# Kernel optimization log

Measured on AMD Instinct MI355X. Metric: run time of the kernel, lower is better.

## Reference

```python
import jax, jax.numpy as jnp
import numpy as np

V, D, H, L, FF, B, S = 32000, 1024, 16, 4, 4096, 2, 1024
DK = D // H
STD = 0.02


def setup_inputs() -> dict:
    key = jax.random.key(0)
    ks = jax.random.split(key, 9)
    emb = jax.random.normal(ks[0], (V, D), jnp.float32) * STD
    w_qkv = jax.random.normal(ks[1], (L, D, 3 * D), jnp.float32) * STD
    w_o = jax.random.normal(ks[2], (L, D, D), jnp.float32) * STD
    w_gate = jax.random.normal(ks[3], (L, D, FF), jnp.float32) * STD
    w_up = jax.random.normal(ks[4], (L, D, FF), jnp.float32) * STD
    w_down = jax.random.normal(ks[5], (L, FF, D), jnp.float32) * STD
    norm1_w = jnp.ones((L, D), jnp.float32)
    norm2_w = jnp.ones((L, D), jnp.float32)
    final_norm_w = jnp.ones((D,), jnp.float32)
    input_ids = jax.random.randint(ks[6], (B, S), 0, V, dtype=jnp.int32)
    return dict(input_ids=input_ids, emb=emb, w_qkv=w_qkv, w_o=w_o,
                norm1_w=norm1_w, norm2_w=norm2_w,
                w_gate=w_gate, w_up=w_up, w_down=w_down,
                final_norm_w=final_norm_w)


def _rms(x, w, eps=1e-8):
    return w * x / jnp.sqrt(jnp.mean(x * x, axis=-1, keepdims=True) + eps)


def _rope_factor(seq_len, dk):
    # original: x_rope = x*cos + x*sin with cos/sin of shape [S, dk/2]
    # (duplicated along the feature dim to make the broadcast well-defined)
    pos = jnp.arange(seq_len, dtype=jnp.float32)
    freqs = jnp.exp(jnp.arange(0, dk, 2, dtype=jnp.float32) * (-jnp.log(10000.0) / dk))
    ang = pos[:, None] * freqs[None, :]                     # [S, dk/2]
    c = jnp.cos(ang); s = jnp.sin(ang)
    return jnp.concatenate([c, c], -1) + jnp.concatenate([s, s], -1)  # [S, dk]


def reference(input_ids, emb, w_qkv, w_o, norm1_w, norm2_w, w_gate, w_up, w_down, final_norm_w):
    b, s = input_ids.shape
    d = emb.shape[1]
    x = emb[input_ids] * jnp.sqrt(jnp.float32(d))           # [B,S,D]
    rope = _rope_factor(s, DK)                              # [S,DK]
    causal = jnp.tril(jnp.ones((s, s), bool))
    scale = 1.0 / jnp.sqrt(jnp.float32(DK))

    def block(x, p):
        wqkv, wo, n1, n2, wg, wu, wd = p
        nx = _rms(x, n1)
        qkv = (nx @ wqkv).reshape(b, s, 3, H, DK).transpose(2, 0, 3, 1, 4)  # [3,B,H,S,DK]
        q, k, v = qkv[0], qkv[1], qkv[2]
        q = q * rope
        k = k * rope
        scores = jnp.einsum('bhsd,bhtd->bhst', q, k) * scale
        scores = jnp.where(causal, scores, jnp.float32(-1e9))
        attn = jax.nn.softmax(scores, axis=-1)
        o = jnp.einsum('bhst,bhtd->bhsd', attn, v)
        o = o.transpose(0, 2, 1, 3).reshape(b, s, d)
        x = x + o @ wo
        nx = _rms(x, n2)
        ff = (jax.nn.silu(nx @ wg) * (nx @ wu)) @ wd
        return x + ff, None

    x, _ = jax.lax.scan(block, x, (w_qkv, w_o, norm1_w, norm2_w, w_gate, w_up, w_down))
    x = _rms(x, final_norm_w)
    logits = x @ emb.T                                      # tied lm_head
    return logits
```

## Files before the change

### kernel.cpp

```cpp
#include <hip/hip_runtime.h>
#include <hip/hip_bf16.h>
#include <math.h>

#define B_ 2
#define S_ 1024
#define D_ 1024
#define H_ 16
#define DK_ 64
#define L_ 4
#define FF_ 4096
#define V_ 32000
#define NT (B_*S_)

typedef __attribute__((ext_vector_type(8))) short short8v;
typedef __attribute__((ext_vector_type(4))) float floatx4;
typedef __hip_bfloat16 bf16;

__device__ inline float b2f(unsigned short u) {
  unsigned v = ((unsigned)u) << 16;
  float f; __builtin_memcpy(&f, &v, 4); return f;
}
__device__ inline unsigned short f2bu(float f) {
  bf16 h = __float2bfloat16(f);
  unsigned short u; __builtin_memcpy(&u, &h, 2); return u;
}

__global__ __launch_bounds__(256) void k_embed(const int* __restrict__ ids,
    const float* __restrict__ emb, float* __restrict__ x) {
  int i = blockIdx.x*256 + threadIdx.x;
  if (i >= NT*D_) return;
  int tok = i >> 10;
  int d = i & 1023;
  x[i] = emb[(size_t)ids[tok]*D_ + d] * 32.0f;
}

__global__ __launch_bounds__(256) void k_rms(const float* __restrict__ x,
    const float* __restrict__ w, bf16* __restrict__ o) {
  int row = blockIdx.x;
  const float* xr = x + (size_t)row*D_;
  float s = 0.f;
  for (int d = threadIdx.x; d < D_; d += 256) { float v = xr[d]; s += v*v; }
  for (int off = 32; off; off >>= 1) s += __shfl_down(s, off);
  __shared__ float red[4];
  __shared__ float inv_s;
  int wid = threadIdx.x >> 6;
  if ((threadIdx.x & 63) == 0) red[wid] = s;
  __syncthreads();
  if (threadIdx.x == 0) {
    float t = red[0]+red[1]+red[2]+red[3];
    inv_s = 1.0f / sqrtf(t * (1.0f/D_) + 1e-8f);
  }
  __syncthreads();
  float inv = inv_s;
  bf16* orow = o + (size_t)row*D_;
  for (int d = threadIdx.x; d < D_; d += 256) orow[d] = __float2bfloat16(w[d]*xr[d]*inv);
}

__global__ __launch_bounds__(256) void k_transpose_cast(const float* __restrict__ src0,
    bf16* __restrict__ dst0, int K, int N, size_t src_stride, size_t dst_stride) {
  const float* src = src0 + blockIdx.z * src_stride;
  bf16* dst = dst0 + blockIdx.z * dst_stride;
  __shared__ float t[64][65];
  int k0 = blockIdx.y*64, n0 = blockIdx.x*64;
  int r  = threadIdx.x >> 4;
  int c4 = (threadIdx.x & 15)*4;
  #pragma unroll
  for (int i = 0; i < 4; ++i) {
    float4 v = *(const float4*)(src + (size_t)(k0 + r + i*16)*N + n0 + c4);
    t[r+i*16][c4] = v.x; t[r+i*16][c4+1] = v.y;
    t[r+i*16][c4+2] = v.z; t[r+i*16][c4+3] = v.w;
  }
  __syncthreads();
  int nn = threadIdx.x >> 2;
  int kc = threadIdx.x & 3;
  #pragma unroll
  for (int i = 0; i < 4; ++i) {
    int kk = kc*4 + i*16;
    ushort4 o;
    o.x = f2bu(t[kk][nn]);   o.y = f2bu(t[kk+1][nn]);
    o.z = f2bu(t[kk+2][nn]); o.w = f2bu(t[kk+3][nn]);
    *(ushort4*)(dst + (size_t)(n0+nn)*K + k0 + kk) = o;
  }
}

__global__ __launch_bounds__(256) void k_cast4(const float* __restrict__ s,
    bf16* __restrict__ d, int n4) {
  int i = blockIdx.x*256 + threadIdx.x;
  if (i >= n4) return;
  float4 v = ((const float4*)s)[i];
  ushort4 o;
  o.x = f2bu(v.x); o.y = f2bu(v.y); o.z = f2bu(v.z); o.w = f2bu(v.w);
  ((ushort4*)d)[i] = o;
}

template<int EPI, bool OUTBF>
__global__ __launch_bounds__(256) void k_mfma_gemm_bt(
    const bf16* __restrict__ A, const bf16* __restrict__ Bt,
    const void* __restrict__ aux, void* __restrict__ Cout,
    int M, int N, int K) {
  const int NM = M >> 7, NN = N >> 7;
  const int wg = blockIdx.x;
  const int grp = wg >> 3, xcd = wg & 7;
  const int mi = grp % NM;
  const int ni = xcd + 8*(grp / NM);
  if (ni >= NN) return;
  const int bm = mi * 128;
  const int bn = ni * 128;

  __shared__ bf16 As[128*32];
  __shared__ bf16 Bs[128*32];
  const int tid  = threadIdx.x;
  const int lane = tid & 63;
  const int wave = tid >> 6;
  const int wm = (wave >> 1) * 64;
  const int wn = (wave & 1) * 64;

  floatx4 acc[4][4] = {};

  for (int k0 = 0; k0 < K; k0 += 32) {
    #pragma unroll
    for (int c = 0; c < 2; ++c) {
      int e = (c*256 + tid) * 8;
      int row = e >> 5, col = e & 31;
      const bf16* ga = A  + (size_t)(bm + row)*K + k0 + col;
      const bf16* gb = Bt + (size_t)(bn + row)*K + k0 + col;
      int ldsoff = (c*256 + wave*64) * 8;
      __builtin_amdgcn_global_load_lds(
        (const __attribute__((address_space(1))) void*)ga,
        (__attribute__((address_space(3))) void*)(As + ldsoff), 16, 0, 0);
      __builtin_amdgcn_global_load_lds(
        (const __attribute__((address_space(1))) void*)gb,
        (__attribute__((address_space(3))) void*)(Bs + ldsoff), 16, 0, 0);
    }
    __syncthreads();
    const int r = lane & 15, kc = lane >> 4;
    short8v a[4], b[4];
    #pragma unroll
    for (int i = 0; i < 4; ++i) {
      a[i] = *(const short8v*)(As + (size_t)(wm + i*16 + r)*32 + kc*8);
      b[i] = *(const short8v*)(Bs + (size_t)(wn + i*16 + r)*32 + kc*8);
    }
    #pragma unroll
    for (int i = 0; i < 4; ++i)
      #pragma unroll
      for (int j = 0; j < 4; ++j)
        acc[i][j] = __builtin_amdgcn_mfma_f32_16x16x32_bf16(a[i], b[j], acc[i][j], 0, 0, 0);
    __syncthreads();
  }

  const int cn = lane & 15, rq = lane >> 4;
  #pragma unroll
  for (int i=0;i<4;i++) {
    #pragma unroll
    for (int j=0;j<4;j++) {
      const int gcol = bn + wn + j*16 + cn;
      float freq = 0.f;
      if constexpr (EPI==2) {
        if (gcol < 2048)
          freq = expf((float)(gcol & 31) * -0.28782313662425574f);
      }
      #pragma unroll
      for (int rr=0; rr<4; ++rr) {
        const int grow = bm + wm + i*16 + rq*4 + rr;
        const size_t off = (size_t)grow*N + gcol;
        float v = acc[i][j][rr];
        if constexpr (EPI==1) v += ((const float*)aux)[off];
        if constexpr (EPI==2) {
          if (gcol < 2048) {
            float sn, cs;
            sincosf((float)(grow & 1023) * freq, &sn, &cs);
            v *= (cs + sn);
          }
        }
        if constexpr (OUTBF) ((bf16*)Cout)[off] = __float2bfloat16(v);
        else                 ((float*)Cout)[off] = v;
      }
    }
  }
}

static inline int remap_grid(int M, int N) {
  int NM = M >> 7, NN = N >> 7;
  int NN8 = (NN + 7) & ~7;
  return NM * NN8;
}

__global__ __launch_bounds__(256) void k_gemm_64(
    const bf16* __restrict__ A, const bf16* __restrict__ Bt,
    const float* __restrict__ res, float* __restrict__ C,
    int M, int N, int K, int lda) {
  const int NN = N >> 7;
  const int nwg = gridDim.x;
  const int id = (blockIdx.x & 7)*(nwg >> 3) + (blockIdx.x >> 3);
  const int mi = id / NN, ni = id % NN;
  const int bm = mi << 6, bn = ni << 7;

  __shared__ bf16 As[64*32];
  __shared__ bf16 Bs[128*32];
  const int tid  = threadIdx.x;
  const int lane = tid & 63;
  const int wave = tid >> 6;
  const int wm = (wave >> 1) * 32;
  const int wn = (wave & 1) * 64;

  floatx4 acc[2][4] = {};

  for (int k0 = 0; k0 < K; k0 += 32) {
    {
      int row = tid >> 2, col = (tid & 3)*8;
      const bf16* ga = A + (size_t)(bm + row)*lda + k0 + col;
      __builtin_amdgcn_global_load_lds(
        (const __attribute__((address_space(1))) void*)ga,
        (__attribute__((address_space(3))) void*)(As + wave*512), 16, 0, 0);
    }
    #pragma unroll
    for (int c = 0; c < 2; ++c) {
      int i = c*256 + tid;
      int row = i >> 2, col = (i & 3)*8;
      const bf16* gb = Bt + (size_t)(bn + row)*K + k0 + col;
      __builtin_amdgcn_global_load_lds(
        (const __attribute__((address_space(1))) void*)gb,
        (__attribute__((address_space(3))) void*)(Bs + (c*256 + wave*64)*8), 16, 0, 0);
    }
    __syncthreads();
    const int r = lane & 15, kc = lane >> 4;
    short8v a[2], b[4];
    #pragma unroll
    for (int i = 0; i < 2; ++i)
      a[i] = *(const short8v*)(As + (size_t)(wm + i*16 + r)*32 + kc*8);
    #pragma unroll
    for (int j = 0; j < 4; ++j)
      b[j] = *(const short8v*)(Bs + (size_t)(wn + j*16 + r)*32 + kc*8);
    #pragma unroll
    for (int i = 0; i < 2; ++i)
      #pragma unroll
      for (int j = 0; j < 4; ++j)
        acc[i][j] = __builtin_amdgcn_mfma_f32_16x16x32_bf16(a[i], b[j], acc[i][j], 0, 0, 0);
    __syncthreads();
  }

  const int cn = lane & 15, rq = lane >> 4;
  #pragma unroll
  for (int i = 0; i < 2; ++i) {
    #pragma unroll
    for (int j = 0; j < 4; ++j) {
      #pragma unroll
      for (int rr = 0; rr < 4; ++rr) {
        int grow = bm + wm + i*16 + rq*4 + rr;
        int gcol = bn + wn + j*16 + cn;
        size_t off = (size_t)grow*N + gcol;
        C[off] = acc[i][j][rr] + res[off];
      }
    }
  }
}

template<bool OUTBF>
__global__ __launch_bounds__(512, 2) void k_gemm256(
    const bf16* __restrict__ A, const bf16* __restrict__ Bt,
    void* __restrict__ C, int M, int N, int K) {
  const int NM = M >> 8;
  const int nwg = gridDim.x;
  const int id = (blockIdx.x & 7)*(nwg >> 3) + (blockIdx.x >> 3);
  const int mi = id % NM, ni = id / NM;
  const int bm = mi << 8, bn = ni << 8;

  __shared__ bf16 As3[3][256*32];
  __shared__ bf16 Bs3[3][256*32];

  const int tid  = threadIdx.x;
  const int lane = tid & 63;
  const int wave = tid >> 6;
  const int wr = wave >> 2;
  const int wc = wave & 3;
  const int fr = lane & 15;
  const int kc = lane >> 4;

  floatx4 acc[8][4] = {};
  const int ntk = K >> 5;

  auto stage_chunk = [&](int kt, int slot, int c) {
    const bf16* Ab = A  + (size_t)bm*K + kt*32;
    const bf16* Bb = Bt + (size_t)bn*K + kt*32;
    int i = c*512 + tid;
    int row = i >> 2, sl = i & 3;
    int gcol = (sl ^ ((row >> 1) & 3)) * 8;
    int ldsoff = (c*512 + wave*64) * 8;
    __builtin_amdgcn_global_load_lds(
      (const __attribute__((address_space(1))) void*)(Ab + (size_t)row*K + gcol),
      (__attribute__((address_space(3))) void*)(&As3[slot][ldsoff]), 16, 0, 0);
    __builtin_amdgcn_global_load_lds(
      (const __attribute__((address_space(1))) void*)(Bb + (size_t)row*K + gcol),
      (__attribute__((address_space(3))) void*)(&Bs3[slot][ldsoff]), 16, 0, 0);
  };

  stage_chunk(0, 0, 0); stage_chunk(0, 0, 1);
  if (ntk > 1) { stage_chunk(1, 1, 0); stage_chunk(1, 1, 1); }

  for (int t = 0; t < ntk; ++t) {
    const int cur = t % 3;
    if (t + 1 < ntk) asm volatile("s_waitcnt vmcnt(4)" ::: "memory");
    else             asm volatile("s_waitcnt vmcnt(0)" ::: "memory");
    __builtin_amdgcn_sched_barrier(0);
    __builtin_amdgcn_s_barrier();
    __builtin_amdgcn_sched_barrier(0);

    const bf16* Ab = As3[cur];
    const bf16* Bb = Bs3[cur];

    short8v a0[4], b[4];
    #pragma unroll
    for (int f = 0; f < 4; ++f) {
      int r = wr*128 + f*16 + fr;
      a0[f] = *(const short8v*)(Ab + r*32 + (kc ^ ((r >> 1) & 3))*8);
    }
    #pragma unroll
    for (int f = 0; f < 4; ++f) {
      int r = wc*64 + f*16 + fr;
      b[f] = *(const short8v*)(Bb + r*32 + (kc ^ ((r >> 1) & 3))*8);
    }
    if (t + 2 < ntk) stage_chunk(t + 2, (t + 2) % 3, 0);
    asm volatile("s_waitcnt lgkmcnt(0)" ::: "memory");
    __builtin_amdgcn_sched_barrier(0);
    __builtin_amdgcn_s_setprio(1);
    #pragma unroll
    for (int f = 0; f < 4; ++f)
      #pragma unroll
      for (int j = 0; j < 4; ++j)
        acc[f][j] = __builtin_amdgcn_mfma_f32_16x16x32_bf16(a0[f], b[j], acc[f][j], 0, 0, 0);
    __builtin_amdgcn_s_setprio(0);
    __builtin_amdgcn_sched_barrier(0);
    __builtin_amdgcn_s_barrier();
    __builtin_amdgcn_sched_barrier(0);

    short8v a1[4];
    #pragma unroll
    for (int f = 0; f < 4; ++f) {
      int r = wr*128 + (f + 4)*16 + fr;
      a1[f] = *(const short8v*)(Ab + r*32 + (kc ^ ((r >> 1) & 3))*8);
    }
    if (t + 2 < ntk) stage_chunk(t + 2, (t + 2) % 3, 1);
    asm volatile("s_waitcnt lgkmcnt(0)" ::: "memory");
    __builtin_amdgcn_sched_barrier(0);
    __builtin_amdgcn_s_setprio(1);
    #pragma unroll
    for (int f = 0; f < 4; ++f)
      #pragma unroll
      for (int j = 0; j < 4; ++j)
        acc[f + 4][j] = __builtin_amdgcn_mfma_f32_16x16x32_bf16(a1[f], b[j], acc[f + 4][j], 0, 0, 0);
    __builtin_amdgcn_s_setprio(0);
    __builtin_amdgcn_sched_barrier(0);
    __builtin_amdgcn_s_barrier();
    __builtin_amdgcn_sched_barrier(0);
  }

  const int cn = lane & 15, rq = lane >> 4;
  #pragma unroll
  for (int f = 0; f < 8; ++f) {
    #pragma unroll
    for (int j = 0; j < 4; ++j) {
      #pragma unroll
      for (int rr = 0; rr < 4; ++rr) {
        int row = bm + wr*128 + f*16 + rq*4 + rr;
        int col = bn + wc*64 + j*16 + cn;
        size_t off = (size_t)row*N + col;
        if constexpr (OUTBF) ((bf16*)C)[off] = __float2bfloat16(acc[f][j][rr]);
        else                 ((float*)C)[off] = acc[f][j][rr];
      }
    }
  }
}

__global__ __launch_bounds__(256) void k_silumul_gu(bf16* __restrict__ gu) {
  int i = blockIdx.x*256 + threadIdx.x;
  if (i >= NT*512) return;
  int row = i >> 9;
  int c8 = (i & 511)*8;
  unsigned short* p = (unsigned short*)gu + (size_t)row*8192 + c8;
  short8v g = *(const short8v*)p;
  short8v u = *(const short8v*)(p + 4096);
  short8v o;
  #pragma unroll
  for (int j = 0; j < 8; ++j) {
    float gf = b2f((unsigned short)g[j]);
    float uf = b2f((unsigned short)u[j]);
    o[j] = (short)f2bu(gf / (1.0f + expf(-gf)) * uf);
  }
  *(short8v*)p = o;
}

__global__ __launch_bounds__(256) void k_vtrans(const bf16* __restrict__ qkvb,
    bf16* __restrict__ vtb) {
  const unsigned short* qkv = (const unsigned short*)qkvb;
  unsigned short* vt = (unsigned short*)vtb;
  const int t0 = blockIdx.x*64, h = blockIdx.y, b = blockIdx.z;
  __shared__ unsigned short t[64][72];
  const int tid = threadIdx.x;
  #pragma unroll
  for (int c = 0; c < 2; ++c) {
    int idx = c*256 + tid;
    int s = idx >> 3, d0 = (idx & 7)*8;
    short8v v = *(const short8v*)(qkv + ((size_t)(b*S_ + t0 + s))*3072 + 2048 + h*DK_ + d0);
    #pragma unroll
    for (int j = 0; j < 8; ++j) t[s][d0+j] = (unsigned short)v[j];
  }
  __syncthreads();
  #pragma unroll
  for (int c = 0; c < 2; ++c) {
    int idx = c*256 + tid;
    int d = idx >> 3, tt0 = (idx & 7)*8;
    short8v o;
    #pragma unroll
    for (int j = 0; j < 8; ++j) o[j] = (short)t[tt0+j][d];
    *(short8v*)(vt + ((size_t)((b*H_ + h)*DK_ + d))*1024 + t0 + tt0) = o;
  }
}

__global__ __launch_bounds__(256) void k_fattn(const bf16* __restrict__ qkvb,
    const bf16* __restrict__ vtb, bf16* __restrict__ outb) {
  const unsigned short* qkv = (const unsigned short*)qkvb;
  const unsigned short* vt  = (const unsigned short*)vtb;
  const int qt = 15 - blockIdx.x;
  const int h = blockIdx.y, b = blockIdx.z;
  const int tid = threadIdx.x, lane = tid & 63, w = tid >> 6;
  const int g = lane >> 4, qn = lane & 15;

  __shared__ unsigned short Ks[2*64*64];
  __shared__ unsigned short Vs[2*64*64];
  __shared__ unsigned short Ps[4*16*64];

  const int q0 = qt * 64;
  const int qw0 = q0 + w*16;

  short8v qf[2];
  {
    const unsigned short* qp = qkv + ((size_t)(b*S_ + qw0 + qn))*3072 + h*DK_ + g*8;
    qf[0] = *(const short8v*)qp;
    qf[1] = *(const short8v*)(qp + 32);
  }

  const int trow = w*8 + (lane>>3);
  const int oct = (lane&7) ^ (trow&7);
  auto stageKV = [&](int it, int buf) {
    const int t0 = it*64;
    #pragma unroll
    for (int c = 0; c < 2; ++c) {
      const unsigned short* gk = qkv + ((size_t)(b*S_ + t0 + c*32 + trow))*3072
                                 + 1024 + h*DK_ + oct*8;
      __builtin_amdgcn_global_load_lds(
        (const __attribute__((address_space(1))) void*)gk,
        (__attribute__((address_space(3))) void*)(Ks + buf*4096 + c*2048 + w*512), 16, 0, 0);
      const unsigned short* gv = vt + ((size_t)((b*H_ + h)*DK_ + c*32 + trow))*1024
                                 + t0 + oct*8;
      __builtin_amdgcn_global_load_lds(
        (const __attribute__((address_space(1))) void*)gv,
        (__attribute__((address_space(3))) void*)(Vs + buf*4096 + c*2048 + w*512), 16, 0, 0);
    }
  };

  floatx4 o_acc[4] = {};
  float m_run = -1e30f, l_run = 0.f;

  const int ntile = qt + 1;
  stageKV(0, 0);
  int cur = 0;

  for (int it = 0; it < ntile; ++it) {
    if (it + 1 < ntile) {
      stageKV(it + 1, cur ^ 1);
      asm volatile("s_waitcnt vmcnt(4)" ::: "memory");
    } else {
      asm volatile("s_waitcnt vmcnt(0)" ::: "memory");
    }
    __builtin_amdgcn_sched_barrier(0);
    __builtin_amdgcn_s_barrier();
    __builtin_amdgcn_sched_barrier(0);

    const unsigned short* Kc = Ks + cur*4096;
    const unsigned short* Vc = Vs + cur*4096;

    floatx4 st[4];
    #pragma unroll
    for (int f = 0; f < 4; ++f) {
      st[f] = (floatx4){0.f,0.f,0.f,0.f};
      int t = f*16 + qn;
      #pragma unroll
      for (int ks = 0; ks < 2; ++ks) {
        int slot = ((ks*4 + g) ^ (t&7)) & 7;
        short8v kf = *(const short8v*)(Kc + t*64 + slot*8);
        st[f] = __builtin_amdgcn_mfma_f32_16x16x32_bf16(kf, qf[ks], st[f], 0,0,0);
      }
    }

    const bool diag = (it == qt);
    float sc[4][4];
    #pragma unroll
    for (int f = 0; f < 4; ++f)
      #pragma unroll
      for (int r = 0; r < 4; ++r) {
        float v = st[f][r]*0.125f;
        if (diag) {
          int tl = f*16 + g*4 + r;
          if (tl > w*16 + qn) v = -1e30f;
        }
        sc[f][r] = v;
      }
    float mx = -1e30f;
    #pragma unroll
    for (int f = 0; f < 4; ++f)
      #pragma unroll
      for (int r = 0; r < 4; ++r) mx = fmaxf(mx, sc[f][r]);
    mx = fmaxf(mx, __shfl_xor(mx, 16));
    mx = fmaxf(mx, __shfl_xor(mx, 32));
    float m_new = fmaxf(m_run, mx);
    float corr = __expf(m_run - m_new);
    m_run = m_new;
    float ls = 0.f;
    #pragma unroll
    for (int f = 0; f < 4; ++f)
      #pragma unroll
      for (int r = 0; r < 4; ++r) {
        float p = __expf(sc[f][r] - m_new);
        sc[f][r] = p;
        ls += p;
      }
    ls += __shfl_xor(ls, 16);
    ls += __shfl_xor(ls, 32);
    l_run = l_run*corr + ls;

    unsigned short* Pw = Ps + w*1024;
    #pragma unroll
    for (int f = 0; f < 4; ++f) {
      unsigned int lo = (unsigned int)f2bu(sc[f][0]) | ((unsigned int)f2bu(sc[f][1]) << 16);
      unsigned int hi = (unsigned int)f2bu(sc[f][2]) | ((unsigned int)f2bu(sc[f][3]) << 16);
      int c16 = f*2 + (g>>1);
      int slot = (c16 ^ (qn&7)) & 7;
      *(uint2*)((char*)Pw + qn*128 + slot*16 + (g&1)*8) = make_uint2(lo, hi);
    }

    #pragma unroll
    for (int r = 0; r < 4; ++r) {
      float cr = __shfl(corr, g*4 + r);
      #pragma unroll
      for (int fd = 0; fd < 4; ++fd) o_acc[fd][r] *= cr;
    }

    short8v pf[2];
    #pragma unroll
    for (int ks = 0; ks < 2; ++ks) {
      int slot = ((ks*4 + g) ^ (qn&7)) & 7;
      pf[ks] = *(const short8v*)(Pw + qn*64 + slot*8);
    }
    #pragma unroll
    for (int fd = 0; fd < 4; ++fd) {
      int d = fd*16 + qn;
      #pragma unroll
      for (int ks = 0; ks < 2; ++ks) {
        int slot = ((ks*4 + g) ^ (d & 7)) & 7;
        short8v vf = *(const short8v*)(Vc + d*64 + slot*8);
        o_acc[fd] = __builtin_amdgcn_mfma_f32_16x16x32_bf16(pf[ks], vf, o_acc[fd], 0,0,0);
      }
    }

    __builtin_amdgcn_sched_barrier(0);
    __builtin_amdgcn_s_barrier();
    __builtin_amdgcn_sched_barrier(0);
    cur ^= 1;
  }

  float linv = 1.0f / l_run;
  #pragma unroll
  for (int r = 0; r < 4; ++r) {
    float li = __shfl(linv, g*4 + r);
    int row = qw0 + g*4 + r;
    bf16* op = outb + (size_t)(b*S_ + row)*D_ + h*DK_ + qn;
    #pragma unroll
    for (int fd = 0; fd < 4; ++fd)
      op[fd*16] = __float2bfloat16(o_acc[fd][r] * li);
  }
}

extern "C" void kernel_launch(void* const* d_in, const int* in_sizes, int n_in,
                              void* d_out, int out_size, void* d_ws, size_t ws_size,
                              hipStream_t stream) {
  (void)in_sizes; (void)n_in; (void)out_size; (void)ws_size;
  const int*   ids  = (const int*)d_in[0];
  const float* emb  = (const float*)d_in[1];
  const float* wqkv = (const float*)d_in[2];
  const float* wo   = (const float*)d_in[3];
  const float* n1   = (const float*)d_in[4];
  const float* n2   = (const float*)d_in[5];
  const float* wg   = (const float*)d_in[6];
  const float* wu   = (const float*)d_in[7];
  const float* wd   = (const float*)d_in[8];
  const float* fnw  = (const float*)d_in[9];
  float* out = (float*)d_out;

  char* ws = (char*)d_ws;
  float* x      = (float*)ws;                                   ws += (size_t)NT*D_*4;
  bf16*  nx_bf  = (bf16*)ws;                                    ws += (size_t)NT*D_*2;
  bf16*  att_bf = (bf16*)ws;                                    ws += (size_t)NT*D_*2;
  bf16*  vt_bf  = (bf16*)ws;                                    ws += (size_t)NT*D_*2;
  bf16*  shared = (bf16*)ws;                                    ws += (size_t)NT*8192*2;
  bf16*  emb_bf = (bf16*)ws;                                    ws += (size_t)V_*D_*2;
  bf16*  qkv_bf = shared;
  bf16*  gu     = shared;

  bf16* wsc = (bf16*)d_out;
  bf16* wqkv_t = wsc;
  bf16* wo_t   = wqkv_t + (size_t)L_*3*D_*D_;
  bf16* wgu_t  = wo_t   + (size_t)L_*D_*D_;
  bf16* wd_t   = wgu_t  + (size_t)L_*2*D_*FF_;

  dim3 blk(256);

  {
    dim3 gq(3*D_/64, D_/64, L_);
    k_transpose_cast<<<gq, blk, 0, stream>>>(wqkv, wqkv_t, D_, 3*D_,
        (size_t)D_*3*D_, (size_t)3*D_*D_);
    dim3 go(D_/64, D_/64, L_);
    k_transpose_cast<<<go, blk, 0, stream>>>(wo, wo_t, D_, D_,
        (size_t)D_*D_, (size_t)D_*D_);
    dim3 gg(FF_/64, D_/64, L_);
    k_transpose_cast<<<gg, blk, 0, stream>>>(wg, wgu_t, D_, FF_,
        (size_t)D_*FF_, (size_t)2*D_*FF_);
    k_transpose_cast<<<gg, blk, 0, stream>>>(wu, wgu_t + (size_t)FF_*D_, D_, FF_,
        (size_t)D_*FF_, (size_t)2*D_*FF_);
    dim3 gdn(D_/64, FF_/64, L_);
    k_transpose_cast<<<gdn, blk, 0, stream>>>(wd, wd_t, FF_, D_,
        (size_t)FF_*D_, (size_t)D_*FF_);
  }
  k_cast4<<<(V_*D_/4 + 255)/256, blk, 0, stream>>>(emb, emb_bf, V_*D_/4);

  k_embed<<<(NT*D_+255)/256, blk, 0, stream>>>(ids, emb, x);

  for (int l = 0; l < L_; ++l) {
    k_rms<<<NT, blk, 0, stream>>>(x, n1 + (size_t)l*D_, nx_bf);
    k_mfma_gemm_bt<2,true><<<remap_grid(NT,3*D_), blk, 0, stream>>>(
        nx_bf, wqkv_t + (size_t)l*3*D_*D_, nullptr, qkv_bf, NT, 3*D_, D_);
    dim3 gvt(S_/64, H_, B_);
    k_vtrans<<<gvt, blk, 0, stream>>>(qkv_bf, vt_bf);
    dim3 gattn(16, H_, B_);
    k_fattn<<<gattn, blk, 0, stream>>>(qkv_bf, vt_bf, att_bf);
    k_gemm_64<<<(NT/64)*(D_/128), blk, 0, stream>>>(
        att_bf, wo_t + (size_t)l*D_*D_, x, x, NT, D_, D_, D_);
    k_rms<<<NT, blk, 0, stream>>>(x, n2 + (size_t)l*D_, nx_bf);
    k_gemm256<true><<<(NT/256)*(2*FF_/256), dim3(512), 0, stream>>>(
        nx_bf, wgu_t + (size_t)l*2*D_*FF_, gu, NT, 2*FF_, D_);
    k_silumul_gu<<<(NT*512 + 255)/256, blk, 0, stream>>>(gu);
    k_gemm_64<<<(NT/64)*(D_/128), blk, 0, stream>>>(
        gu, wd_t + (size_t)l*D_*FF_, x, x, NT, D_, FF_, 2*FF_);
  }
  k_rms<<<NT, blk, 0, stream>>>(x, fnw, nx_bf);
  k_gemm256<false><<<(NT/256)*(V_/256), dim3(512), 0, stream>>>(
      nx_bf, emb_bf, out, NT, V_, D_);
}
```

Measured before the change: 1.273 ms.

## Double-buffer LDS tiles in k_gemm_64 to overlap global loads with MFMA

Turns the 64x128 GEMM's shared-memory tiles into two buffers and prefetches the next K-slice with global_load_lds while the current one is multiplied. Partial vmcnt waits and raw s_barrier replace the full syncthreads wait, and s_setprio raises priority around the MFMA block. The goal is to hide global-to-LDS latency that was previously serialized with compute, at the cost of twice the LDS per block, which may reduce occupancy.

Result: no change. 1.269 ms, median of 2 (-0.3%).

```diff
diff --git a/kernel.cpp b/kernel.cpp
--- a/kernel.cpp
+++ b/kernel.cpp
@@ -195,8 +195,8 @@
   const int mi = id / NN, ni = id % NN;
   const int bm = mi << 6, bn = ni << 7;
 
-  __shared__ bf16 As[64*32];
-  __shared__ bf16 Bs[128*32];
+  __shared__ bf16 As2[2][64*32];
+  __shared__ bf16 Bs2[2][128*32];
   const int tid  = threadIdx.x;
   const int lane = tid & 63;
   const int wave = tid >> 6;
@@ -204,39 +204,62 @@
   const int wn = (wave & 1) * 64;
 
   floatx4 acc[2][4] = {};
-
-  for (int k0 = 0; k0 < K; k0 += 32) {
+  const int ntk = K >> 5;
+
+  auto stage = [&](int kt, int buf) {
     {
       int row = tid >> 2, col = (tid & 3)*8;
-      const bf16* ga = A + (size_t)(bm + row)*lda + k0 + col;
+      const bf16* ga = A + (size_t)(bm + row)*lda + kt*32 + col;
       __builtin_amdgcn_global_load_lds(
         (const __attribute__((address_space(1))) void*)ga,
-        (__attribute__((address_space(3))) void*)(As + wave*512), 16, 0, 0);
+        (__attribute__((address_space(3))) void*)(As2[buf] + wave*512), 16, 0, 0);
     }
     #pragma unroll
     for (int c = 0; c < 2; ++c) {
       int i = c*256 + tid;
       int row = i >> 2, col = (i & 3)*8;
-      const bf16* gb = Bt + (size_t)(bn + row)*K + k0 + col;
+      const bf16* gb = Bt + (size_t)(bn + row)*K + kt*32 + col;
       __builtin_amdgcn_global_load_lds(
         (const __attribute__((address_space(1))) void*)gb,
-        (__attribute__((address_space(3))) void*)(Bs + (c*256 + wave*64)*8), 16, 0, 0);
-    }
-    __syncthreads();
+        (__attribute__((address_space(3))) void*)(Bs2[buf] + (c*256 + wave*64)*8), 16, 0, 0);
+    }
+  };
+
+  stage(0, 0);
+  int buf = 0;
+  for (int t = 0; t < ntk; ++t) {
+    if (t + 1 < ntk) {
+      stage(t + 1, buf ^ 1);
+      asm volatile("s_waitcnt vmcnt(3)" ::: "memory");
+    } else {
+      asm volatile("s_waitcnt vmcnt(0)" ::: "memory");
+    }
+    __builtin_amdgcn_sched_barrier(0);
+    __builtin_amdgcn_s_barrier();
+    __builtin_amdgcn_sched_barrier(0);
+
+    const bf16* Ab = As2[buf];
+    const bf16* Bb = Bs2[buf];
     const int r = lane & 15, kc = lane >> 4;
     short8v a[2], b[4];
     #pragma unroll
     for (int i = 0; i < 2; ++i)
-      a[i] = *(const short8v*)(As + (size_t)(wm + i*16 + r)*32 + kc*8);
+      a[i] = *(const short8v*)(Ab + (size_t)(wm + i*16 + r)*32 + kc*8);
     #pragma unroll
     for (int j = 0; j < 4; ++j)
-      b[j] = *(const short8v*)(Bs + (size_t)(wn + j*16 + r)*32 + kc*8);
+      b[j] = *(const short8v*)(Bb + (size_t)(wn + j*16 + r)*32 + kc*8);
+    __builtin_amdgcn_s_setprio(1);
     #pragma unroll
     for (int i = 0; i < 2; ++i)
       #pragma unroll
       for (int j = 0; j < 4; ++j)
         acc[i][j] = __builtin_amdgcn_mfma_f32_16x16x32_bf16(a[i], b[j], acc[i][j], 0, 0, 0);
-    __syncthreads();
+    __builtin_amdgcn_s_setprio(0);
+
+    __builtin_amdgcn_sched_barrier(0);
+    __builtin_amdgcn_s_barrier();
+    __builtin_amdgcn_sched_barrier(0);
+    buf ^= 1;
   }
 
   const int cn = lane & 15, rq = lane >> 4;
```
